# Kernel optimization log

Hardware: AMD Instinct MI355X
Metric: run time of the kernel (lower is better)

Reference implementation:

```python
import jax, jax.numpy as jnp
import numpy as np

LMAX = 3
KMAX = [128, 96, 64, 32]   # k_max_l, decreasing in l
N_ATOMS = 10000
N_EDGES = 100000
N_RADIAL = 8
CUTOFF = 5.0

def _bounds(l):
    lo = KMAX[l + 1] if l < LMAX else 0
    return lo, KMAX[l]

def _uncouple(split_list, U):
    # split_list: per l' in 0..L, [n, 2l'+1, k]; U: [3**L, (L+1)**2]
    x = jnp.concatenate(split_list, axis=1)      # [n, (L+1)**2, k]
    return jnp.einsum('dm,nmk->ndk', U, x)       # [n, 3**L, k]

def _couple(f, U, L):
    x = jnp.einsum('dm,ndk->nmk', U, f)          # [n, (L+1)**2, k]
    out, off = [], 0
    for lp in range(L + 1):
        out.append(x[:, off:off + 2 * lp + 1, :])
        off += 2 * lp + 1
    return out

def _forward(r, sh, feat, Wrad, U, Wlin, centers, neighbors):
    # radial basis with smooth cutoff, then per-l channel embedding
    n = jnp.arange(1, N_RADIAL + 1, dtype=r.dtype)
    rb = jnp.sin(n * jnp.pi * r[:, None] / CUTOFF) / (r[:, None] + 1e-6)
    fc = 0.5 * (jnp.cos(jnp.pi * jnp.clip(r / CUTOFF, 0.0, 1.0)) + 1.0)
    rb = rb * fc[:, None]                        # [E, N_RADIAL]
    radial = [rb @ Wrad[l] for l in range(LMAX + 1)]          # [E, KMAX[l]]
    vexp = [sh[l] * radial[l][:, None, :] for l in range(LMAX + 1)]  # [E, 2l+1, KMAX[l]]

    def group(ts, l):
        lo, hi = _bounds(l)
        return [ts[lp][:, :, lo:hi] for lp in range(l + 1)]

    unc_v = [_uncouple(group(vexp, l), U[l]) for l in range(LMAX + 1)]
    unc_f = [_uncouple(group(feat, l), U[l]) for l in range(LMAX + 1)]
    # neighbor gather + elementwise combine in the uncoupled (Cartesian) space
    combined = [unc_v[l] * unc_f[l][neighbors] for l in range(LMAX + 1)]
    # scatter-add pooling over centers (index_add_ equivalent)
    pooled = [jax.ops.segment_sum(c, centers, num_segments=N_ATOMS) for c in combined]
    coupled = [_couple(pooled[l], U[l], l) for l in range(LMAX + 1)]
    cat = [jnp.concatenate([coupled[lp][l] for lp in range(l, LMAX + 1)], axis=-1)
           for l in range(LMAX + 1)]             # [n_atoms, 2l+1, KMAX[l]]
    # NOTE: mp_scaling multiply in the original is dead code (result unused)
    out = [feat[l] + jnp.einsum('nmk,kq->nmq', cat[l], Wlin[l]) for l in range(LMAX + 1)]
    return tuple(out)

def setup_inputs() -> dict:
    key = jax.random.key(0)
    ks = jax.random.split(key, 40)
    inp = {'r': jax.random.uniform(ks[0], (N_EDGES,), minval=0.5, maxval=CUTOFF, dtype=jnp.float32)}
    for l in range(LMAX + 1):
        k = KMAX[l]
        inp[f'sh{l}'] = jax.random.normal(ks[1 + l], (N_EDGES, 2 * l + 1, 1), dtype=jnp.float32)
        inp[f'feat{l}'] = jax.random.normal(ks[5 + l], (N_ATOMS, 2 * l + 1, k), dtype=jnp.float32)
        inp[f'Wrad{l}'] = jax.random.normal(ks[9 + l], (N_RADIAL, k), dtype=jnp.float32) / np.sqrt(N_RADIAL).astype(np.float32)
        inp[f'U{l}'] = jax.random.normal(ks[13 + l], (3 ** l, (l + 1) ** 2), dtype=jnp.float32) / np.float32(np.sqrt((l + 1) ** 2))
        inp[f'Wlin{l}'] = jax.random.normal(ks[17 + l], (k, k), dtype=jnp.float32) / np.sqrt(k).astype(np.float32)
    inp['centers'] = jax.random.randint(ks[21], (N_EDGES,), 0, N_ATOMS, dtype=jnp.int32)
    inp['neighbors'] = jax.random.randint(ks[22], (N_EDGES,), 0, N_ATOMS, dtype=jnp.int32)
    return inp

def reference(r, sh0, sh1, sh2, sh3, feat0, feat1, feat2, feat3,
              Wrad0, Wrad1, Wrad2, Wrad3, U0, U1, U2, U3,
              Wlin0, Wlin1, Wlin2, Wlin3, centers, neighbors):
    return _forward(r, [sh0, sh1, sh2, sh3], [feat0, feat1, feat2, feat3],
                    [Wrad0, Wrad1, Wrad2, Wrad3], [U0, U1, U2, U3],
                    [Wlin0, Wlin1, Wlin2, Wlin3], centers, neighbors)
```

## Files before the change

kernel.cpp:

```cpp
#include <hip/hip_runtime.h>
#include <hip/hip_fp16.h>
#include <math.h>

#define NA 10000
#define NE 100000
#define PI_F 3.14159265358979323846f


__device__ __forceinline__ constexpr int rowC(int row) {
    return (row == 0) ? 0 : (row < 4) ? 1 : (row < 13) ? 2 : 3;
}

__device__ __forceinline__ void stage_U(const float* __restrict__ U0,
                                        const float* __restrict__ U1,
                                        const float* __restrict__ U2,
                                        const float* __restrict__ U3,
                                        float* uLds, int t, int nthr) {
    for (int i = t; i < 526; i += nthr) {
        float v;
        if (i == 0)       v = U0[0];
        else if (i < 13)  v = U1[i - 1];
        else if (i < 94)  v = U2[i - 13];
        else              v = U3[i - 94];
        uLds[i] = v;
    }
}

__global__ __launch_bounds__(256) void kCount(const int* __restrict__ centers,
                                              int* __restrict__ counts)
{
    const int e = blockIdx.x * 256 + threadIdx.x;
    if (e < NE) atomicAdd(&counts[centers[e]], 1);
}

__global__ __launch_bounds__(1024) void kScan(const int* __restrict__ counts,
                                              int* __restrict__ offsets,
                                              int* __restrict__ cursor)
{
    __shared__ int sums[1024];
    const int t = threadIdx.x;
    const int base = t * 10;
    int local[10];
    int s = 0;
#pragma unroll
    for (int j = 0; j < 10; ++j) {
        int idx = base + j;
        int v = (idx < NA) ? counts[idx] : 0;
        local[j] = s;
        s += v;
    }
    sums[t] = s;
    __syncthreads();
    for (int off = 1; off < 1024; off <<= 1) {
        int v = (t >= off) ? sums[t - off] : 0;
        __syncthreads();
        sums[t] += v;
        __syncthreads();
    }
    const int prev = (t == 0) ? 0 : sums[t - 1];
#pragma unroll
    for (int j = 0; j < 10; ++j) {
        int idx = base + j;
        if (idx <= NA) {
            int o = prev + local[j];
            offsets[idx] = o;
            if (idx < NA) cursor[idx] = o;
        }
    }
}

__global__ __launch_bounds__(256) void kPrep(
    const float* __restrict__ f0, const float* __restrict__ f1,
    const float* __restrict__ f2, const float* __restrict__ f3,
    const float* __restrict__ r,
    const float* __restrict__ sh0, const float* __restrict__ sh1,
    const float* __restrict__ sh2, const float* __restrict__ sh3,
    const float* __restrict__ U0, const float* __restrict__ U1,
    const float* __restrict__ U2, const float* __restrict__ U3,
    const int* __restrict__ centers, const int* __restrict__ neighbors,
    int* __restrict__ cursor,
    uint4* __restrict__ uncf16, float* __restrict__ rbbuf,
    float* __restrict__ csbuf, int* __restrict__ nbrs)
{
    __shared__ float uLds[526];
    const int t = threadIdx.x;
    stage_U(U0, U1, U2, U3, uLds, t, 256);
    __syncthreads();

    if (blockIdx.x < 1250) {
        const int la = t >> 5, k = t & 31;
        const int a = blockIdx.x * 8 + la;
        float arr[40];

        {
            arr[0] = uLds[0] * f0[(size_t)a * 128 + 96 + k];
        }
        {
            float x[4];
            x[0] = f0[(size_t)a * 128 + 64 + k];
#pragma unroll
            for (int m = 0; m < 3; ++m) x[1 + m] = f1[(size_t)a * 288 + m * 96 + 64 + k];
#pragma unroll
            for (int d = 0; d < 3; ++d) {
                float acc = 0.f;
#pragma unroll
                for (int m = 0; m < 4; ++m) acc += uLds[1 + d * 4 + m] * x[m];
                arr[1 + d] = acc;
            }
        }
        {
            float x[9];
            x[0] = f0[(size_t)a * 128 + 32 + k];
#pragma unroll
            for (int m = 0; m < 3; ++m) x[1 + m] = f1[(size_t)a * 288 + m * 96 + 32 + k];
#pragma unroll
            for (int m = 0; m < 5; ++m) x[4 + m] = f2[(size_t)a * 320 + m * 64 + 32 + k];
#pragma unroll
            for (int d = 0; d < 9; ++d) {
                float acc = 0.f;
#pragma unroll
                for (int m = 0; m < 9; ++m) acc += uLds[13 + d * 9 + m] * x[m];
                arr[4 + d] = acc;
            }
        }
        {
            float x[16];
            x[0] = f0[(size_t)a * 128 + k];
#pragma unroll
            for (int m = 0; m < 3; ++m) x[1 + m] = f1[(size_t)a * 288 + m * 96 + k];
#pragma unroll
            for (int m = 0; m < 5; ++m) x[4 + m] = f2[(size_t)a * 320 + m * 64 + k];
#pragma unroll
            for (int m = 0; m < 7; ++m) x[9 + m] = f3[(size_t)a * 224 + m * 32 + k];
#pragma unroll
            for (int d = 0; d < 27; ++d) {
                float acc = 0.f;
#pragma unroll
                for (int m = 0; m < 16; ++m) acc += uLds[94 + d * 16 + m] * x[m];
                arr[13 + d] = acc;
            }
        }
        uint4* op = uncf16 + (size_t)a * 160 + k;
#pragma unroll
        for (int jj = 0; jj < 5; ++jj) {
            uint4 w;
            __half2 h0 = __floats2half2_rn(arr[8 * jj + 0], arr[8 * jj + 1]);
            __half2 h1 = __floats2half2_rn(arr[8 * jj + 2], arr[8 * jj + 3]);
            __half2 h2 = __floats2half2_rn(arr[8 * jj + 4], arr[8 * jj + 5]);
            __half2 h3 = __floats2half2_rn(arr[8 * jj + 6], arr[8 * jj + 7]);
            w.x = *(unsigned int*)&h0; w.y = *(unsigned int*)&h1;
            w.z = *(unsigned int*)&h2; w.w = *(unsigned int*)&h3;
            op[jj * 32] = w;
        }
    } else {
        const int e = (blockIdx.x - 1250) * 256 + t;
        if (e >= NE) return;

        const int c_ = centers[e];
        const int pos = atomicAdd(&cursor[c_], 1);
        nbrs[pos] = neighbors[e];

        float shv[16];
        shv[0] = sh0[e];
#pragma unroll
        for (int m = 0; m < 3; ++m) shv[1 + m] = sh1[(size_t)e * 3 + m];
#pragma unroll
        for (int m = 0; m < 5; ++m) shv[4 + m] = sh2[(size_t)e * 5 + m];
#pragma unroll
        for (int m = 0; m < 7; ++m) shv[9 + m] = sh3[(size_t)e * 7 + m];

        const float rv = r[e];
        const float fc = 0.5f * (cosf(PI_F * fminf(rv * 0.2f, 1.0f)) + 1.0f);
        const float pref = fc / (rv + 1e-6f);
        const float step = rv * (PI_F * 0.2f);
        float4 ra, rb;
        ra.x = sinf(1.f * step) * pref; ra.y = sinf(2.f * step) * pref;
        ra.z = sinf(3.f * step) * pref; ra.w = sinf(4.f * step) * pref;
        rb.x = sinf(5.f * step) * pref; rb.y = sinf(6.f * step) * pref;
        rb.z = sinf(7.f * step) * pref; rb.w = sinf(8.f * step) * pref;
        *(float4*)(rbbuf + (size_t)pos * 8)     = ra;
        *(float4*)(rbbuf + (size_t)pos * 8 + 4) = rb;

        const int UO[4] = {0, 1, 13, 94};
        const int RO[4] = {0, 1, 4, 13};
        const int P3[4] = {1, 3, 9, 27};
        float4* cso = (float4*)csbuf + (size_t)pos * 40;
#pragma unroll
        for (int c = 0; c < 4; ++c) {
            const int M2 = (c + 1) * (c + 1);
            for (int d = 0; d < P3[c]; ++d) {
                float4 cv = make_float4(0.f, 0.f, 0.f, 0.f);
                float* cvp = &cv.x;
#pragma unroll
                for (int lp = 0; lp < 4; ++lp) {
                    if (lp > c) break;
                    float s = 0.f;
#pragma unroll
                    for (int ml = 0; ml < 2 * lp + 1; ++ml)
                        s += uLds[UO[c] + d * M2 + lp * lp + ml] * shv[lp * lp + ml];
                    cvp[lp] = s;
                }
                cso[RO[c] + d] = cv;
            }
        }
    }
}

__global__ __launch_bounds__(256, 2) void kB2(
    const float* __restrict__ Wr0, const float* __restrict__ Wr1,
    const float* __restrict__ Wr2, const float* __restrict__ Wr3,
    const int* __restrict__ offsets, const int* __restrict__ nbrs,
    const float* __restrict__ rbbuf, const float* __restrict__ csbuf,
    const uint4* __restrict__ uncf16, float* __restrict__ pooled)
{
    __shared__ float wLds[2560];
    const int t = threadIdx.x;
    for (int i = t; i < 2560; i += 256) {
        float v;
        if (i < 1024)      v = Wr0[i];
        else if (i < 1792) v = Wr1[i - 1024];
        else if (i < 2304) v = Wr2[i - 1792];
        else               v = Wr3[i - 2304];
        wLds[i] = v;
    }
    __syncthreads();

    const int lane = t & 63;
    const int wv = t >> 6;
    const int k = lane & 31;
    const int g2 = lane >> 5;
    const int a = blockIdx.x * 4 + wv;
    const int beg = offsets[a], end = offsets[a + 1];

    float acc[40];
#pragma unroll
    for (int i = 0; i < 40; ++i) acc[i] = 0.f;

    const int KL[4] = {128, 96, 64, 32};
    const int WO[4] = {0, 1024, 1792, 2304};

    int i = beg + g2;
    int nbr = (i < end) ? nbrs[i] : 0;
    for (; i < end; i += 2) {
        const int nbr_nx = (i + 2 < end) ? nbrs[i + 2] : 0;

        const uint4* up = uncf16 + (size_t)nbr * 160 + k;
        const uint4 w0 = up[0 * 32];
        const uint4 w1 = up[1 * 32];
        const uint4 w2 = up[2 * 32];
        const uint4 w3 = up[3 * 32];
        const uint4 w4 = up[4 * 32];

        const float4 r0 = *(const float4*)(rbbuf + (size_t)i * 8);
        const float4 r1 = *(const float4*)(rbbuf + (size_t)i * 8 + 4);
        const float rb[8] = {r0.x, r0.y, r0.z, r0.w, r1.x, r1.y, r1.z, r1.w};

        float rad[4][4];
#pragma unroll
        for (int lp = 0; lp < 4; ++lp) {
#pragma unroll
            for (int c = 0; c < 4; ++c) {
                if (c < lp) continue;
                const int base = 32 * (3 - c);
                float s = 0.f;
#pragma unroll
                for (int n = 0; n < 8; ++n)
                    s += rb[n] * wLds[WO[lp] + n * KL[lp] + base + k];
                rad[lp][c] = s;
            }
        }

        const float4* cs = (const float4*)csbuf + (size_t)i * 40;
        const uint4 ww[5] = {w0, w1, w2, w3, w4};
#pragma unroll
        for (int jj = 0; jj < 5; ++jj) {
            const unsigned int ws[4] = {ww[jj].x, ww[jj].y, ww[jj].z, ww[jj].w};
#pragma unroll
            for (int p2 = 0; p2 < 4; ++p2) {
                const int row0 = 8 * jj + 2 * p2, row1 = row0 + 1;
                const int c0 = rowC(row0), c1 = rowC(row1);
                const __half2 h = *(const __half2*)&ws[p2];
                const float4 cva = cs[row0];
                const float4 cvb = cs[row1];
                float uv0 = cva.x * rad[0][c0];
                if (c0 >= 1) uv0 += cva.y * rad[1][c0];
                if (c0 >= 2) uv0 += cva.z * rad[2][c0];
                if (c0 >= 3) uv0 += cva.w * rad[3][c0];
                float uv1 = cvb.x * rad[0][c1];
                if (c1 >= 1) uv1 += cvb.y * rad[1][c1];
                if (c1 >= 2) uv1 += cvb.z * rad[2][c1];
                if (c1 >= 3) uv1 += cvb.w * rad[3][c1];
                acc[row0] += uv0 * __low2float(h);
                acc[row1] += uv1 * __high2float(h);
            }
        }
        nbr = nbr_nx;
    }

#pragma unroll
    for (int row = 0; row < 40; ++row) acc[row] += __shfl_xor(acc[row], 32);

    float* pp = pooled + (size_t)a * 1280 + k;
#pragma unroll
    for (int rr = 0; rr < 20; ++rr) {
        const float v   = g2 ? acc[rr + 20] : acc[rr];
        const int  row  = g2 ? (rr + 20)    : rr;
        pp[row * 32] = v;
    }
}

__global__ __launch_bounds__(256) void kC_out(
    const float* __restrict__ pooled,
    const float* __restrict__ f0, const float* __restrict__ f1,
    const float* __restrict__ f2, const float* __restrict__ f3,
    const float* __restrict__ U0, const float* __restrict__ U1,
    const float* __restrict__ U2, const float* __restrict__ U3,
    const float* __restrict__ W0, const float* __restrict__ W1,
    const float* __restrict__ W2, const float* __restrict__ W3,
    float* __restrict__ out)
{
    __shared__ float uLds[526];
    __shared__ float plds[4 * 1280];
    __shared__ float clds[120 * 33];
    const int t = threadIdx.x;
    stage_U(U0, U1, U2, U3, uLds, t, 256);
    const int a0 = blockIdx.x * 4;
    {
        const float4* src = (const float4*)(pooled + (size_t)a0 * 1280);
        float4* dst = (float4*)plds;
        for (int i = t; i < 1280; i += 256) dst[i] = src[i];
    }
    __syncthreads();

    if (t < 128) {
        const int la = t >> 5, kk = t & 31;
        clds[(la * 30 + 0) * 33 + kk] = uLds[0] * plds[la * 1280 + 0 * 32 + kk];
    }
#pragma unroll
    for (int s = t; s < 512; s += 256) {
        const int la = s >> 7, rem = s & 127;
        const int m = rem >> 5, kk = rem & 31;
        float acc = 0.f;
#pragma unroll
        for (int d = 0; d < 3; ++d)
            acc += uLds[1 + d * 4 + m] * plds[la * 1280 + (1 + d) * 32 + kk];
        clds[(la * 30 + 1 + m) * 33 + kk] = acc;
    }
    for (int s = t; s < 1152; s += 256) {
        const int la = s / 288, rem = s - la * 288;
        const int m = rem >> 5, kk = rem & 31;
        float acc = 0.f;
#pragma unroll
        for (int d = 0; d < 9; ++d)
            acc += uLds[13 + d * 9 + m] * plds[la * 1280 + (4 + d) * 32 + kk];
        clds[(la * 30 + 5 + m) * 33 + kk] = acc;
    }
    for (int s = t; s < 2048; s += 256) {
        const int la = s >> 9, rem = s & 511;
        const int m = rem >> 5, kk = rem & 31;
        float acc = 0.f;
#pragma unroll
        for (int d = 0; d < 27; ++d)
            acc += uLds[94 + d * 16 + m] * plds[la * 1280 + (13 + d) * 32 + kk];
        clds[(la * 30 + 14 + m) * 33 + kk] = acc;
    }
    __syncthreads();

    int l, m, q;
    bool active = true;
    if (t < 32)       { l = 0; m = 0;                               q = 4 * t; }
    else if (t < 104) { l = 1; int u = t - 32;  m = u / 24; q = 4 * (u % 24); }
    else if (t < 184) { l = 2; int u = t - 104; m = u / 16; q = 4 * (u % 16); }
    else if (t < 240) { l = 3; int u = t - 184; m = u / 8;  q = 4 * (u % 8);  }
    else active = false;

    if (active) {
        const int K  = (l == 0) ? 128 : (l == 1) ? 96 : (l == 2) ? 64 : 32;
        const int MK = (l == 0) ? 128 : (l == 1) ? 288 : (l == 2) ? 320 : 224;
        const size_t Ol = (l == 0) ? 0 : (l == 1) ? 1280000 : (l == 2) ? 4160000 : 7360000;
        const float* F = (l == 0) ? f0 : (l == 1) ? f1 : (l == 2) ? f2 : f3;
        const float* W = (l == 0) ? W0 : (l == 1) ? W1 : (l == 2) ? W2 : W3;
        const int CRB[4] = {0, 1, 5, 14};

        float4 acc[4];
#pragma unroll
        for (int la = 0; la < 4; ++la)
            acc[la] = *(const float4*)(F + (size_t)(a0 + la) * MK + m * K + q);

        for (int j = 0; j < 4 - l; ++j) {
            const int c = l + j;
            const int crow = CRB[c] + l * l + m;
#pragma unroll
            for (int kk = 0; kk < 32; ++kk) {
                const float4 w = *(const float4*)(W + (size_t)(32 * j + kk) * K + q);
#pragma unroll
                for (int la = 0; la < 4; ++la) {
                    const float cv = clds[(la * 30 + crow) * 33 + kk];
                    acc[la].x += cv * w.x; acc[la].y += cv * w.y;
                    acc[la].z += cv * w.z; acc[la].w += cv * w.w;
                }
            }
        }
#pragma unroll
        for (int la = 0; la < 4; ++la)
            *(float4*)(out + Ol + (size_t)(a0 + la) * MK + m * K + q) = acc[la];
    }
}

extern "C" void kernel_launch(void* const* d_in, const int* in_sizes, int n_in,
                              void* d_out, int out_size, void* d_ws, size_t ws_size,
                              hipStream_t stream)
{
    int ir, ish[4], ift[4], iwr[4], iu[4], iwl[4], ic, in_;
    if (in_sizes[2] == 300000) {
        ir = 0;
        for (int l = 0; l < 4; ++l) { ish[l] = 1 + l; ift[l] = 5 + l; iwr[l] = 9 + l; iu[l] = 13 + l; iwl[l] = 17 + l; }
        ic = 21; in_ = 22;
    } else {
        ir = 0;
        for (int l = 0; l < 4; ++l) { ish[l] = 1 + 5 * l; ift[l] = 2 + 5 * l; iwr[l] = 3 + 5 * l; iu[l] = 4 + 5 * l; iwl[l] = 5 + 5 * l; }
        ic = 21; in_ = 22;
    }
    const float* r   = (const float*)d_in[ir];
    const float* sh0 = (const float*)d_in[ish[0]];
    const float* sh1 = (const float*)d_in[ish[1]];
    const float* sh2 = (const float*)d_in[ish[2]];
    const float* sh3 = (const float*)d_in[ish[3]];
    const float* f0  = (const float*)d_in[ift[0]];
    const float* f1  = (const float*)d_in[ift[1]];
    const float* f2  = (const float*)d_in[ift[2]];
    const float* f3  = (const float*)d_in[ift[3]];
    const float* Wr0 = (const float*)d_in[iwr[0]];
    const float* Wr1 = (const float*)d_in[iwr[1]];
    const float* Wr2 = (const float*)d_in[iwr[2]];
    const float* Wr3 = (const float*)d_in[iwr[3]];
    const float* U0  = (const float*)d_in[iu[0]];
    const float* U1  = (const float*)d_in[iu[1]];
    const float* U2  = (const float*)d_in[iu[2]];
    const float* U3  = (const float*)d_in[iu[3]];
    const float* Wl0 = (const float*)d_in[iwl[0]];
    const float* Wl1 = (const float*)d_in[iwl[1]];
    const float* Wl2 = (const float*)d_in[iwl[2]];
    const float* Wl3 = (const float*)d_in[iwl[3]];
    const int* centers   = (const int*)d_in[ic];
    const int* neighbors = (const int*)d_in[in_];

    uint4* uncf16 = (uint4*)d_ws;
    float* pooled = (float*)(uncf16 + (size_t)NA * 160);
    float* rbbuf  = pooled + (size_t)NA * 1280;
    float* csbuf  = rbbuf + (size_t)NE * 8;
    int*   nbrs    = (int*)(csbuf + (size_t)NE * 160);
    int*   counts  = nbrs + NE;
    int*   offsets = counts + NA;
    int*   cursor  = offsets + NA + 1;
    float* outp   = (float*)d_out;

    hipMemsetAsync(counts, 0, NA * sizeof(int), stream);
    kCount<<<(NE + 255) / 256, 256, 0, stream>>>(centers, counts);
    kScan<<<1, 1024, 0, stream>>>(counts, offsets, cursor);
    kPrep<<<1250 + (NE + 255) / 256, 256, 0, stream>>>(
        f0, f1, f2, f3, r, sh0, sh1, sh2, sh3, U0, U1, U2, U3,
        centers, neighbors, cursor, uncf16, rbbuf, csbuf, nbrs);
    kB2<<<NA / 4, 256, 0, stream>>>(Wr0, Wr1, Wr2, Wr3, offsets, nbrs,
                                    rbbuf, csbuf, uncf16, pooled);
    kC_out<<<NA / 4, 256, 0, stream>>>(pooled, f0, f1, f2, f3, U0, U1, U2, U3,
                                       Wl0, Wl1, Wl2, Wl3, outp);
}
```

Before: 355.4 us.

## Store per-edge coupling coefficients in fp16 and fuse count with scan kernel

Per-edge coupling coefficients (40 rows of 4 values) are now stored as packed half precision instead of float4, halving that buffer's write traffic in kPrep and read traffic in kB2. Separately, the edge-count histogram moves into the single-block scan kernel using LDS atomics, which removes a memset and a kernel launch. The cost is reduced precision on the coefficients, and a single block now serially processes all 100k edges for counting.

```diff
diff --git a/kernel.cpp b/kernel.cpp
--- a/kernel.cpp
+++ b/kernel.cpp
@@ -26,26 +26,25 @@
     }
 }
 
-__global__ __launch_bounds__(256) void kCount(const int* __restrict__ centers,
-                                              int* __restrict__ counts)
+__global__ __launch_bounds__(1024) void kCountScan(
+    const int* __restrict__ centers,
+    int* __restrict__ offsets, int* __restrict__ cursor)
 {
-    const int e = blockIdx.x * 256 + threadIdx.x;
-    if (e < NE) atomicAdd(&counts[centers[e]], 1);
-}
-
-__global__ __launch_bounds__(1024) void kScan(const int* __restrict__ counts,
-                                              int* __restrict__ offsets,
-                                              int* __restrict__ cursor)
-{
+    __shared__ int cnt[NA];
     __shared__ int sums[1024];
     const int t = threadIdx.x;
+    for (int i = t; i < NA; i += 1024) cnt[i] = 0;
+    __syncthreads();
+    for (int e = t; e < NE; e += 1024) atomicAdd(&cnt[centers[e]], 1);
+    __syncthreads();
+
     const int base = t * 10;
     int local[10];
     int s = 0;
 #pragma unroll
     for (int j = 0; j < 10; ++j) {
         int idx = base + j;
-        int v = (idx < NA) ? counts[idx] : 0;
+        int v = (idx < NA) ? cnt[idx] : 0;
         local[j] = s;
         s += v;
     }
@@ -80,7 +79,7 @@
     const int* __restrict__ centers, const int* __restrict__ neighbors,
     int* __restrict__ cursor,
     uint4* __restrict__ uncf16, float* __restrict__ rbbuf,
-    float* __restrict__ csbuf, int* __restrict__ nbrs)
+    uint2* __restrict__ csh, int* __restrict__ nbrs)
 {
     __shared__ float uLds[526];
     const int t = threadIdx.x;
@@ -184,13 +183,12 @@
         const int UO[4] = {0, 1, 13, 94};
         const int RO[4] = {0, 1, 4, 13};
         const int P3[4] = {1, 3, 9, 27};
-        float4* cso = (float4*)csbuf + (size_t)pos * 40;
+        uint2* cso = csh + (size_t)pos * 40;
 #pragma unroll
         for (int c = 0; c < 4; ++c) {
             const int M2 = (c + 1) * (c + 1);
             for (int d = 0; d < P3[c]; ++d) {
-                float4 cv = make_float4(0.f, 0.f, 0.f, 0.f);
-                float* cvp = &cv.x;
+                float cv[4] = {0.f, 0.f, 0.f, 0.f};
 #pragma unroll
                 for (int lp = 0; lp < 4; ++lp) {
                     if (lp > c) break;
@@ -198,9 +196,14 @@
 #pragma unroll
                     for (int ml = 0; ml < 2 * lp + 1; ++ml)
                         s += uLds[UO[c] + d * M2 + lp * lp + ml] * shv[lp * lp + ml];
-                    cvp[lp] = s;
+                    cv[lp] = s;
                 }
-                cso[RO[c] + d] = cv;
+                __half2 h0 = __floats2half2_rn(cv[0], cv[1]);
+                __half2 h1 = __floats2half2_rn(cv[2], cv[3]);
+                uint2 u;
+                u.x = *(unsigned int*)&h0;
+                u.y = *(unsigned int*)&h1;
+                cso[RO[c] + d] = u;
             }
         }
     }
@@ -210,7 +213,7 @@
     const float* __restrict__ Wr0, const float* __restrict__ Wr1,
     const float* __restrict__ Wr2, const float* __restrict__ Wr3,
     const int* __restrict__ offsets, const int* __restrict__ nbrs,
-    const float* __restrict__ rbbuf, const float* __restrict__ csbuf,
+    const float* __restrict__ rbbuf, const uint2* __restrict__ csh,
     const uint4* __restrict__ uncf16, float* __restrict__ pooled)
 {
     __shared__ float wLds[2560];
@@ -270,7 +273,7 @@
             }
         }
 
-        const float4* cs = (const float4*)csbuf + (size_t)i * 40;
+        const uint2* cs = csh + (size_t)i * 40;
         const uint4 ww[5] = {w0, w1, w2, w3, w4};
 #pragma unroll
         for (int jj = 0; jj < 5; ++jj) {
@@ -280,16 +283,20 @@
                 const int row0 = 8 * jj + 2 * p2, row1 = row0 + 1;
                 const int c0 = rowC(row0), c1 = rowC(row1);
                 const __half2 h = *(const __half2*)&ws[p2];
-                const float4 cva = cs[row0];
-                const float4 cvb = cs[row1];
-                float uv0 = cva.x * rad[0][c0];
-                if (c0 >= 1) uv0 += cva.y * rad[1][c0];
-                if (c0 >= 2) uv0 += cva.z * rad[2][c0];
-                if (c0 >= 3) uv0 += cva.w * rad[3][c0];
-                float uv1 = cvb.x * rad[0][c1];
-                if (c1 >= 1) uv1 += cvb.y * rad[1][c1];
-                if (c1 >= 2) uv1 += cvb.z * rad[2][c1];
-                if (c1 >= 3) uv1 += cvb.w * rad[3][c1];
+                const uint2 ua = cs[row0];
+                const uint2 ub = cs[row1];
+                const __half2 a01 = *(const __half2*)&ua.x;
+                const __half2 a23 = *(const __half2*)&ua.y;
+                const __half2 b01 = *(const __half2*)&ub.x;
+                const __half2 b23 = *(const __half2*)&ub.y;
+                float uv0 = __low2float(a01) * rad[0][c0];
+                if (c0 >= 1) uv0 += __high2float(a01) * rad[1][c0];
+                if (c0 >= 2) uv0 += __low2float(a23) * rad[2][c0];
+                if (c0 >= 3) uv0 += __high2float(a23) * rad[3][c0];
+                float uv1 = __low2float(b01) * rad[0][c1];
+                if (c1 >= 1) uv1 += __high2float(b01) * rad[1][c1];
+                if (c1 >= 2) uv1 += __low2float(b23) * rad[2][c1];
+                if (c1 >= 3) uv1 += __high2float(b23) * rad[3][c1];
                 acc[row0] += uv0 * __low2float(h);
                 acc[row1] += uv1 * __high2float(h);
             }
@@ -448,21 +455,18 @@
     uint4* uncf16 = (uint4*)d_ws;
     float* pooled = (float*)(uncf16 + (size_t)NA * 160);
     float* rbbuf  = pooled + (size_t)NA * 1280;
-    float* csbuf  = rbbuf + (size_t)NE * 8;
-    int*   nbrs    = (int*)(csbuf + (size_t)NE * 160);
-    int*   counts  = nbrs + NE;
-    int*   offsets = counts + NA;
+    uint2* csh    = (uint2*)(rbbuf + (size_t)NE * 8);
+    int*   nbrs    = (int*)(csh + (size_t)NE * 40);
+    int*   offsets = nbrs + NE;
     int*   cursor  = offsets + NA + 1;
     float* outp   = (float*)d_out;
 
-    hipMemsetAsync(counts, 0, NA * sizeof(int), stream);
-    kCount<<<(NE + 255) / 256, 256, 0, stream>>>(centers, counts);
-    kScan<<<1, 1024, 0, stream>>>(counts, offsets, cursor);
+    kCountScan<<<1, 1024, 0, stream>>>(centers, offsets, cursor);
     kPrep<<<1250 + (NE + 255) / 256, 256, 0, stream>>>(
         f0, f1, f2, f3, r, sh0, sh1, sh2, sh3, U0, U1, U2, U3,
-        centers, neighbors, cursor, uncf16, rbbuf, csbuf, nbrs);
+        centers, neighbors, cursor, uncf16, rbbuf, csh, nbrs);
     kB2<<<NA / 4, 256, 0, stream>>>(Wr0, Wr1, Wr2, Wr3, offsets, nbrs,
-                                    rbbuf, csbuf, uncf16, pooled);
+                                    rbbuf, csh, uncf16, pooled);
     kC_out<<<NA / 4, 256, 0, stream>>>(pooled, f0, f1, f2, f3, U0, U1, U2, U3,
                                        Wl0, Wl1, Wl2, Wl3, outp);
 }
```

After: 364.0 us. 2.4% more time.
